# Performance work log

Measured on AMD Instinct MI355X. Metric: run time of the kernel, lower is better.

## Reference

```python
import jax, jax.numpy as jnp
import numpy as np

CANVAS = 512
SCORE_THR = 0.02
NMS_THR = 0.45
LVTOP = 1000      # cfg['lvtop'] for mm source
IMTOP = 200       # cfg['imtop']
NMS_PRE = 2000    # fixed pre-NMS candidate cap (static shape for jit)
NUM_CLASSES = 80
STRIDES = [8, 16, 32, 64, 128, 256, 512]
AR3 = [False, True, True, True, True, False, False]


def _make_priors():
    # get_scales(512): smallest=0.04, rmin=0.1, rmax=0.9, n=7
    smallest, rmin, rmax, n = 0.04, 0.1, 0.9, 7
    step = (rmax - rmin) / (n - 2)
    scales = [smallest] + [rmin + i * step for i in range(n)]
    sz = np.round(np.array(scales) * CANVAS).astype(np.int64)
    pr, lvlen = [], []
    for i, s in enumerate(STRIDES):
        fs = CANVAS // s
        ratios = [1.0, 2.0, 0.5] + ([3.0, 1.0 / 3.0] if AR3[i] else [])
        wh = [(sz[i] * np.sqrt(r), sz[i] / np.sqrt(r)) for r in ratios]
        extra = np.sqrt(float(sz[i]) * float(sz[i + 1]))  # sqrt(sz[i+1]/sz[i])*sz[i]
        wh.insert(1, (extra, extra))
        wh = np.array(wh, np.float32)            # [na, 2]
        xs = (np.arange(fs, dtype=np.float32) + 0.5) * s
        cx, cy = np.meshgrid(xs, xs)             # rows index y
        ctr = np.stack([cx, cy], -1)[:, :, None, :]  # [fs, fs, 1, 2]
        na = wh.shape[0]
        p = np.concatenate([np.broadcast_to(ctr, (fs, fs, na, 2)),
                            np.broadcast_to(wh, (fs, fs, na, 2))], -1).reshape(-1, 4)
        pr.append(p)
        lvlen.append(p.shape[0])
    return np.concatenate(pr).astype(np.float32), lvlen

PRIORS_NP, LVLEN = _make_priors()   # total 24564, lvlen=[16384,6144,1536,384,96,16,4]


def setup_inputs() -> dict:
    key = jax.random.key(0)
    k1, k2 = jax.random.split(key)
    A = PRIORS_NP.shape[0]
    cls_logits = jax.random.normal(k1, (4, A, NUM_CLASSES + 1), dtype=jnp.float32)
    reg = jax.random.normal(k2, (4, A, 4), dtype=jnp.float32)
    priors = jnp.asarray(PRIORS_NP)
    return {"cls_logits": cls_logits, "reg": reg, "priors": priors}


def _pairwise_iou(b):  # b: [K,4] xyxy
    area = (b[:, 2] - b[:, 0]) * (b[:, 3] - b[:, 1])
    lt = jnp.maximum(b[:, None, :2], b[None, :, :2])
    rb = jnp.minimum(b[:, None, 2:], b[None, :, 2:])
    wh = jnp.clip(rb - lt, 0.0)
    inter = wh[..., 0] * wh[..., 1]
    return inter / jnp.maximum(area[:, None] + area[None, :] - inter, 1e-6)


def _nms_keep(b):  # boxes sorted by descending score, class-offset applied
    m = _pairwise_iou(b) * jnp.triu(jnp.ones((NMS_PRE, NMS_PRE), b.dtype), 1)
    def body(sup, i):
        sup = sup | ((~sup[i]) & (m[i] > NMS_THR))
        return sup, None
    sup, _ = jax.lax.scan(body, jnp.zeros((NMS_PRE,), bool), jnp.arange(NMS_PRE))
    return ~sup


def reference(cls_logits, reg, priors):
    N = cls_logits.shape[0]
    C = NUM_CLASSES
    # softmax, background class is LAST (bckg_class_first=False for mm source)
    scr = jax.nn.softmax(cls_logits, axis=-1)[..., :-1]
    scr = jnp.where(scr > SCORE_THR, scr, 0.0)  # score threshold (fidx filter)
    # per-level top-k over flattened (anchor, class) pairs  [post.top_per_level]
    vals_l, anch_l, cls_l = [], [], []
    start = 0
    for lv in LVLEN:
        f = scr[:, start:start + lv, :].reshape(N, lv * C)
        k = min(LVTOP, lv * C)
        v, idx = jax.lax.top_k(f, k)
        vals_l.append(v)
        anch_l.append(start + idx // C)
        cls_l.append(idx % C)
        start += lv
    vals = jnp.concatenate(vals_l, 1)
    anch = jnp.concatenate(anch_l, 1)
    cls = jnp.concatenate(cls_l, 1)
    # fixed-size pre-NMS cap (static shapes under jit)
    v2, sel = jax.lax.top_k(vals, NMS_PRE)
    anch = jnp.take_along_axis(anch, sel, 1)
    cls = jnp.take_along_axis(cls, sel, 1)
    # decode boxes  [post.decode_boxes, mults=(0.1, 0.2), clamp=True]
    p = priors[anch]                                 # [N,K,4] cxcywh
    r = jnp.take_along_axis(reg, anch[..., None], 1)  # [N,K,4]
    cx = p[..., 0] + r[..., 0] * 0.1 * p[..., 2]
    cy = p[..., 1] + r[..., 1] * 0.1 * p[..., 3]
    w = p[..., 2] * jnp.exp(r[..., 2] * 0.2)
    h = p[..., 3] * jnp.exp(r[..., 3] * 0.2)
    boxes = jnp.stack([cx - w / 2, cy - h / 2, cx + w / 2, cy + h / 2], -1)
    boxes = jnp.clip(boxes, 0.0, float(CANVAS))
    # class-aware NMS via class offsets
    nb = boxes + cls.astype(boxes.dtype)[..., None] * (2.0 * CANVAS)
    keep = jax.vmap(_nms_keep)(nb)                   # [N,K] bool
    fs = jnp.where(keep & (v2 > 0), v2, 0.0)
    fv, fi = jax.lax.top_k(fs, IMTOP)                # imtop
    fb = jnp.take_along_axis(boxes, fi[..., None], 1)
    fc = jnp.take_along_axis(cls, fi, 1)
    fb = jnp.where(fv[..., None] > 0, fb, 0.0)
    return fb, fv, fc
```

## Files before the change

kernel.cpp:

```cpp
#include <hip/hip_runtime.h>
#include <hip/hip_bf16.h>
#include <math.h>

typedef unsigned long long u64;
typedef unsigned int u32;

#define A_TOTAL 24564
#define NCLS 80
#define NIMG 4
#define NPRE 2000
#define NLV 7
#define HBUCKETS 1024
#define BEXP_BASE 0x3CA3
#define TOTAL_G (NIMG * A_TOTAL)
#define FA 64
#define FT 256
#define NBLK_F ((TOTAL_G + FA - 1) / FA)
#define POOL_CAP_MAX 4096
#define CAPSEL 4608

__device__ __constant__ int c_klv[NLV] = {1000,1000,1000,1000,1000,1000,320};

#define WS_HIST      0
#define WS_MCOUNT    114688
#define WS_BCOUNT    114800
#define WS_ZERO_END  114912
#define WS_PCOUNT    114912
#define WS_CUTS      121056
#define WS_MAIN      121280
#define WS_BND       350656
#define WS_BOXES     1268160
#define WS_CLS       1396160
#define WS_SCORE     1428160
#define WS_MASK      1460160
#define WS_POOL      3508160

#define NZERO_W (WS_ZERO_END / 4)

__device__ inline u64 shfl_u64(u64 v, int src) {
  int lo = __shfl((int)(u32)(v & 0xFFFFFFFFULL), src);
  int hi = __shfl((int)(u32)(v >> 32), src);
  return ((u64)(u32)hi << 32) | (u32)lo;
}

__device__ inline int score_bucket(u32 bits) {
  int b = (int)(bits >> 16) - BEXP_BASE;
  return b < 0 ? 0 : (b > HBUCKETS - 1 ? HBUCKETS - 1 : b);
}

__device__ inline int level_of(int a) {
  return (a < 16384) ? 0 : (a < 22528) ? 1 : (a < 24064) ? 2 :
         (a < 24448) ? 3 : (a < 24544) ? 4 : (a < 24560) ? 5 : 6;
}

__global__ __launch_bounds__(256) void k_zero(u32* __restrict__ p) {
  int i = blockIdx.x * 256 + threadIdx.x;
  if (i < NZERO_W) p[i] = 0;
}

__device__ inline void wave_find_cut(const u32* __restrict__ h, int k, int lane,
                                     int& cx, int& cy) {
  u32 s = 0;
#pragma unroll
  for (int i = 0; i < 16; ++i) s += h[lane * 16 + i];
  u32 S = s;
#pragma unroll
  for (int o = 1; o < 64; o <<= 1) {
    u32 t = (u32)__shfl_down((int)S, o);
    if (lane + o < 64) S += t;
  }
  u32 total = (u32)__shfl((int)S, 0);
  if (total <= (u32)k) { cx = -1; cy = 0; return; }
  u64 bm = __ballot(S >= (u32)k);
  int L0 = 63 - (int)__clzll((long long)bm);
  u32 Sup = (u32)__shfl_down((int)S, 1);
  if (lane == 63) Sup = 0;
  int rcx = 0, rcy = 0;
  if (lane == L0) {
    u32 cum = Sup;
    for (int i = 15; i >= 0; --i) {
      u32 c = h[lane * 16 + i];
      if (cum + c >= (u32)k) { rcx = lane * 16 + i; rcy = k - (int)cum; break; }
      cum += c;
    }
  }
  cx = __shfl(rcx, L0);
  cy = __shfl(rcy, L0);
}

__global__ __launch_bounds__(FT) void k_fused(const float* __restrict__ logits,
                                              u32* __restrict__ histG,
                                              u64* __restrict__ pool,
                                              u32* __restrict__ pcount, int cap) {
  __shared__ float sx[FA * 81];
  __shared__ u32 sh[HBUCKETS];
  __shared__ int nm;
  int tid = threadIdx.x, bx = blockIdx.x;
  for (int b = tid; b < HBUCKETS; b += FT) sh[b] = 0;
  if (tid == 0) nm = 0;
  size_t base_f = (size_t)bx * (FA * 81);
  int cap4 = FA * 81 / 4;
  long long rem4 = ((long long)TOTAL_G * 81 - (long long)base_f) / 4;
  int n4 = (rem4 > cap4) ? cap4 : (int)rem4;
  const float4* src = (const float4*)(logits + base_f);
  float4* dst = (float4*)sx;
  for (int t = tid; t < n4; t += FT) dst[t] = src[t];
  __syncthreads();
  int la = tid >> 2, q = tid & 3;
  int g = bx * FA + la;
  bool valid = g < TOTAL_G;
  int g0 = bx * FA;
  int seg0 = (g0 / A_TOTAL) * NLV + level_of(g0 % A_TOTAL);
  int seg = seg0, a = 0;
  float e[20];
  float rt = 0.f;
  if (valid) {
    int img = g / A_TOTAL;
    a = g - img * A_TOTAL;
    seg = img * NLV + level_of(a);
    int rowoff = la * 81, c0 = q * 20;
    float mloc = sx[rowoff + c0];
#pragma unroll
    for (int i = 1; i < 20; ++i) mloc = fmaxf(mloc, sx[rowoff + c0 + i]);
    if (q == 3) mloc = fmaxf(mloc, sx[rowoff + 80]);
    float m = fmaxf(mloc, __shfl_xor(mloc, 1));
    m = fmaxf(m, __shfl_xor(m, 2));
    float tq = 0.f;
#pragma unroll
    for (int i = 0; i < 20; ++i) { e[i] = expf(sx[rowoff + c0 + i] - m); tq += e[i]; }
    if (q == 3) tq += expf(sx[rowoff + 80] - m);
    float t = tq + __shfl_xor(tq, 1);
    t = t + __shfl_xor(t, 2);
    rt = 1.0f / t;
  }
  int uniform = __syncthreads_and((int)(!valid || seg == seg0));
  if (valid) {
    u32* hdst = uniform ? sh : (histG + (size_t)seg * HBUCKETS);
    int c0 = q * 20;
    u32 wmask = 0;
#pragma unroll
    for (int i = 0; i < 20; ++i) {
      float s = e[i] * rt;
      if (s > 0.02f) wmask |= (1u << i);
    }
    int cnt = __popc(wmask);
    int basep = 0;
    if (cnt) basep = atomicAdd(&nm, cnt);
    while (wmask) {
      int i = __ffs(wmask) - 1;
      wmask &= wmask - 1;
      float s = e[i] * rt;
      u32 bits = __float_as_uint(s);
      atomicAdd(&hdst[score_bucket(bits)], 1u);
      if (basep < cap)
        pool[(size_t)bx * cap + basep] =
            ((u64)bits << 32) | (u64)(0xFFFFFFFFu - (u32)(a * NCLS + c0 + i));
      ++basep;
    }
  }
  __syncthreads();
  if (uniform) {
    u32* hseg = histG + (size_t)seg0 * HBUCKETS;
    for (int b = tid; b < HBUCKETS; b += FT) {
      u32 v = sh[b];
      if (v) atomicAdd(&hseg[b], v);
    }
  }
  if (tid == 0) pcount[bx] = (u32)nm;
}

__global__ __launch_bounds__(1024) void k_cuts(const u32* __restrict__ histG,
                                               int2* __restrict__ cutsG) {
  int wid = threadIdx.x >> 6, lane = threadIdx.x & 63;
  for (int seg = wid; seg < NIMG * NLV; seg += 16) {
    int cx, cy;
    wave_find_cut(histG + (size_t)seg * HBUCKETS, c_klv[seg % NLV], lane, cx, cy);
    if (lane == 0) cutsG[seg] = make_int2(cx, cy);
  }
}

__global__ __launch_bounds__(FT) void k_filter(const float* __restrict__ logits,
                                               const u64* __restrict__ pool,
                                               const u32* __restrict__ pcount,
                                               const int2* __restrict__ cutsG, int cap,
                                               u64* __restrict__ mainG, u32* __restrict__ mcount,
                                               u64* __restrict__ bndG, u32* __restrict__ bcount) {
  __shared__ float sx[FA * 81];
  __shared__ int2 scuts[NIMG * NLV];
  __shared__ u64 mk[1024]; __shared__ unsigned char msg_[1024];
  __shared__ u64 bkl[256]; __shared__ unsigned char bsg[256];
  __shared__ int nm, nb, cm[4], cb[4], basem[4], baseb[4], wm[4], wb[4];
  int tid = threadIdx.x, bx = blockIdx.x;
  if (tid < NIMG * NLV) scuts[tid] = cutsG[tid];
  if (tid < 4) { cm[tid] = 0; cb[tid] = 0; wm[tid] = 0; wb[tid] = 0; }
  if (tid == 0) { nm = 0; nb = 0; }
  int g0 = bx * FA;
  int img0 = g0 / A_TOTAL;
  int alo = g0 - img0 * A_TOTAL;
  int gN = g0 + FA - 1; if (gN > TOTAL_G - 1) gN = TOTAL_G - 1;
  int seg_lo = img0 * NLV + level_of(alo);
  int seg_hi = (gN / A_TOTAL) * NLV + level_of(gN % A_TOTAL);
  __syncthreads();
  int n = (int)pcount[bx];
  if (n <= cap) {
    for (int t = tid; t < n; t += FT) {
      u64 key = pool[(size_t)bx * cap + t];
      u32 bits = (u32)(key >> 32);
      u32 flat = 0xFFFFFFFFu - (u32)(key & 0xFFFFFFFFULL);
      int a = (int)(flat / NCLS);
      int img = (a >= alo) ? img0 : img0 + 1;
      int seg = img * NLV + level_of(a);
      int2 ct = scuts[seg];
      int bk = score_bucket(bits);
      int si = seg - seg_lo;
      if (ct.x < 0 || bk > ct.x) {
        int p = atomicAdd(&nm, 1);
        if (p < 1024) { mk[p] = key; msg_[p] = (unsigned char)si; atomicAdd(&cm[si], 1); }
        else { u32 pg = atomicAdd(&mcount[seg], 1u); if (pg < 1024) mainG[(size_t)seg * 1024 + pg] = key; }
      } else if (bk == ct.x) {
        int p = atomicAdd(&nb, 1);
        if (p < 256) { bkl[p] = key; bsg[p] = (unsigned char)si; atomicAdd(&cb[si], 1); }
        else { u32 pg = atomicAdd(&bcount[seg], 1u); if (pg < 4096) bndG[(size_t)seg * 4096 + pg] = key; }
      }
    }
  } else {
    size_t base_f = (size_t)bx * (FA * 81);
    int cap4 = FA * 81 / 4;
    long long rem4 = ((long long)TOTAL_G * 81 - (long long)base_f) / 4;
    int n4 = (rem4 > cap4) ? cap4 : (int)rem4;
    const float4* src = (const float4*)(logits + base_f);
    float4* dst = (float4*)sx;
    for (int t = tid; t < n4; t += FT) dst[t] = src[t];
    __syncthreads();
    int la = tid >> 2, q = tid & 3;
    int g = g0 + la;
    if (g < TOTAL_G) {
      int img = g / A_TOTAL;
      int a = g - img * A_TOTAL;
      int seg = img * NLV + level_of(a);
      int si = seg - seg_lo;
      int2 ct = scuts[seg];
      int rowoff = la * 81, c0 = q * 20;
      float mloc = sx[rowoff + c0];
#pragma unroll
      for (int i = 1; i < 20; ++i) mloc = fmaxf(mloc, sx[rowoff + c0 + i]);
      if (q == 3) mloc = fmaxf(mloc, sx[rowoff + 80]);
      float m = fmaxf(mloc, __shfl_xor(mloc, 1));
      m = fmaxf(m, __shfl_xor(m, 2));
      float tq = 0.f;
      float e[20];
#pragma unroll
      for (int i = 0; i < 20; ++i) { e[i] = expf(sx[rowoff + c0 + i] - m); tq += e[i]; }
      if (q == 3) tq += expf(sx[rowoff + 80] - m);
      float tt = tq + __shfl_xor(tq, 1);
      tt = tt + __shfl_xor(tt, 2);
      float rt = 1.0f / tt;
      for (int i = 0; i < 20; ++i) {
        float s = e[i] * rt;
        if (s > 0.02f) {
          u32 bits = __float_as_uint(s);
          int bk = score_bucket(bits);
          u64 key = ((u64)bits << 32) | (u64)(0xFFFFFFFFu - (u32)(a * NCLS + c0 + i));
          if (ct.x < 0 || bk > ct.x) {
            int p = atomicAdd(&nm, 1);
            if (p < 1024) { mk[p] = key; msg_[p] = (unsigned char)si; atomicAdd(&cm[si], 1); }
            else { u32 pg = atomicAdd(&mcount[seg], 1u); if (pg < 1024) mainG[(size_t)seg * 1024 + pg] = key; }
          } else if (bk == ct.x) {
            int p = atomicAdd(&nb, 1);
            if (p < 256) { bkl[p] = key; bsg[p] = (unsigned char)si; atomicAdd(&cb[si], 1); }
            else { u32 pg = atomicAdd(&bcount[seg], 1u); if (pg < 4096) bndG[(size_t)seg * 4096 + pg] = key; }
          }
        }
      }
    }
  }
  __syncthreads();
  if (tid <= seg_hi - seg_lo) {
    if (cm[tid] > 0) basem[tid] = (int)atomicAdd(&mcount[seg_lo + tid], (u32)cm[tid]);
    if (cb[tid] > 0) baseb[tid] = (int)atomicAdd(&bcount[seg_lo + tid], (u32)cb[tid]);
  }
  __syncthreads();
  int tm = nm < 1024 ? nm : 1024;
  for (int idx = tid; idx < tm; idx += FT) {
    int si = msg_[idx];
    int slot = atomicAdd(&wm[si], 1);
    int d = basem[si] + slot;
    if (d < 1024) mainG[(size_t)(seg_lo + si) * 1024 + d] = mk[idx];
  }
  int tb = nb < 256 ? nb : 256;
  for (int idx = tid; idx < tb; idx += FT) {
    int si = bsg[idx];
    int slot = atomicAdd(&wb[si], 1);
    int d = baseb[si] + slot;
    if (d < 4096) bndG[(size_t)(seg_lo + si) * 4096 + d] = bkl[idx];
  }
}

__device__ inline void bitonic_desc(u64* s, int n) {
  for (int k = 2; k <= n; k <<= 1)
    for (int j = k >> 1; j > 0; j >>= 1) {
      __syncthreads();
      for (int i = threadIdx.x; i < n; i += blockDim.x) {
        int l = i ^ j;
        if (l > i) {
          u64 a = s[i], b = s[l];
          if (((i & k) == 0) ? (a < b) : (a > b)) { s[i] = b; s[l] = a; }
        }
      }
    }
  __syncthreads();
}

__global__ __launch_bounds__(1024) void k_refine(const u32* __restrict__ histG,
                                                 const u64* __restrict__ bndG,
                                                 const u32* __restrict__ bcount,
                                                 u64* __restrict__ mainG, u32* __restrict__ mcount) {
  int seg = blockIdx.x;
  __shared__ int sh_cx, sh_cy;
  __shared__ u64 s[4096];
  int tid = threadIdx.x, lane = tid & 63;
  if (tid < 64) {
    int cx, cy;
    wave_find_cut(histG + (size_t)seg * HBUCKETS, c_klv[seg % NLV], lane, cx, cy);
    if (lane == 0) { sh_cx = cx; sh_cy = cy; }
  }
  __syncthreads();
  if (sh_cx < 0) return;
  int m = (int)bcount[seg]; if (m > 4096) m = 4096;
  int n = 64; while (n < m) n <<= 1;
  for (int t = tid; t < n; t += 1024)
    s[t] = (t < m) ? bndG[(size_t)seg * 4096 + t] : 0ULL;
  bitonic_desc(s, n);
  int kp = sh_cy; if (kp > m) kp = m;
  int base = (int)mcount[seg];
  for (int t = tid; t < kp; t += 1024) {
    int p = base + t;
    if (p < 1024) mainG[(size_t)seg * 1024 + p] = s[t];
  }
  __syncthreads();
  if (tid == 0) {
    int nb = base + kp;
    mcount[seg] = (u32)(nb > 1024 ? 1024 : nb);
  }
}

__global__ __launch_bounds__(1024) void k_gsel(const u32* __restrict__ histG,
                                               const u64* __restrict__ mainG,
                                               const u32* __restrict__ mcount,
                                               const float4* __restrict__ priors,
                                               const float4* __restrict__ reg,
                                               float4* __restrict__ boxesG,
                                               int* __restrict__ clsG,
                                               float* __restrict__ scoreG) {
  int img = blockIdx.x;
  int tid = threadIdx.x, wid = tid >> 6, lane = tid & 63;
  __shared__ u32 H[HBUCKETS];
  __shared__ u32 cntb[HBUCKETS];
  __shared__ u32 Sarr[HBUCKETS];
  __shared__ u32 cnt2[HBUCKETS];
  __shared__ u64 sel[CAPSEL];
  __shared__ int lcx[NLV], lcy[NLV];
  __shared__ int sh_gx, sh_gy, sh_cC, sh_cand, sh_sgx;
  if (tid == 0) { sh_cC = 0; sh_cand = 0; sh_sgx = -1; }
  if (wid < NLV) {
    int cx, cy;
    wave_find_cut(histG + (size_t)(img * NLV + wid) * HBUCKETS, c_klv[wid], lane, cx, cy);
    if (lane == 0) { lcx[wid] = cx; lcy[wid] = cy; }
  }
  __syncthreads();
  for (int b = tid; b < HBUCKETS; b += 1024) {
    u32 acc = 0;
#pragma unroll
    for (int l = 0; l < NLV; ++l) {
      u32 h = histG[(size_t)(img * NLV + l) * HBUCKETS + b];
      int cx = lcx[l];
      if (cx < 0 || b > cx) acc += h;
      else if (b == cx) acc += (u32)lcy[l];
    }
    H[b] = acc;
    cntb[b] = 0;
    cnt2[b] = 0;
  }
  __syncthreads();
  if (wid == 0) {
    int gx, gy;
    wave_find_cut(H, NPRE, lane, gx, gy);
    if (lane == 0) { sh_gx = gx; sh_gy = gy; }
  }
  __syncthreads();
  int gx = sh_gx, gy = sh_gy;
  int mcap[NLV];
#pragma unroll
  for (int l = 0; l < NLV; ++l) { int c = (int)mcount[img * NLV + l]; mcap[l] = c > 1024 ? 1024 : c; }
  for (int l = 0; l < NLV; ++l)
    for (int t = tid; t < mcap[l]; t += 1024) {
      u64 key = mainG[(size_t)(img * NLV + l) * 1024 + t];
      int b = score_bucket((u32)(key >> 32));
      if (gx < 0 || b > gx) atomicAdd(&cntb[b], 1u);
      else if (b == gx) atomicAdd(&sh_cC, 1);
    }
  __syncthreads();
  for (int b = tid; b < HBUCKETS; b += 1024) Sarr[b] = cntb[b];
  __syncthreads();
  {
    u32* A = Sarr; u32* B = H;
    for (int o = 1; o < HBUCKETS; o <<= 1) {
      for (int b = tid; b < HBUCKETS; b += 1024)
        B[b] = A[b] + ((b + o < HBUCKETS) ? A[b + o] : 0u);
      __syncthreads();
      u32* tmp = A; A = B; B = tmp;
    }
  }
  int cA = (int)Sarr[0];
  int cC = sh_cC;
  int cand = (gx >= 0) ? cC : 0;
  int sgx = -1;
  if (gx >= 0 && cA + cC > CAPSEL) {
    for (int b = tid; b < HBUCKETS; b += 1024) H[b] = 0;
    __syncthreads();
    for (int l = 0; l < NLV; ++l)
      for (int t = tid; t < mcap[l]; t += 1024) {
        u64 key = mainG[(size_t)(img * NLV + l) * 1024 + t];
        u32 bits = (u32)(key >> 32);
        if (score_bucket(bits) == gx) atomicAdd(&H[(bits >> 6) & 1023], 1u);
      }
    __syncthreads();
    if (wid == 0) {
      int a1, a2;
      wave_find_cut(H, gy, lane, a1, a2);
      if (lane == 0) sh_sgx = a1;
    }
    __syncthreads();
    sgx = sh_sgx;
    if (sgx >= 0) {
      for (int s2 = tid; s2 < HBUCKETS; s2 += 1024)
        if (s2 >= sgx) { u32 v = H[s2]; if (v) atomicAdd(&sh_cand, (int)v); }
      __syncthreads();
      cand = sh_cand;
    }
    if (cA + cand > CAPSEL) cand = CAPSEL - cA;
  }
  __syncthreads();
  for (int l = 0; l < NLV; ++l)
    for (int t = tid; t < mcap[l]; t += 1024) {
      u64 key = mainG[(size_t)(img * NLV + l) * 1024 + t];
      u32 bits = (u32)(key >> 32);
      int b = score_bucket(bits);
      bool inc = false; int segbase = 0, seglen = 0;
      if (gx < 0 || b > gx) {
        inc = true; segbase = (int)(Sarr[b] - cntb[b]); seglen = (int)cntb[b];
      } else if (b == gx) {
        inc = (sgx < 0) || ((int)((bits >> 6) & 1023) >= sgx);
        segbase = (int)Sarr[b]; seglen = cand;
      }
      if (inc) {
        int slot = (int)atomicAdd(&cnt2[b], 1u);
        if (slot < seglen) sel[segbase + slot] = key;
      }
    }
  __syncthreads();
  int total = cA + cand;
  u64 myk[5]; int myp[5];
#pragma unroll
  for (int it = 0; it < 5; ++it) {
    int t = tid + it * 1024;
    myp[it] = -1; myk[it] = 0;
    if (t < total) {
      u64 key = sel[t];
      u32 bits = (u32)(key >> 32);
      int b = score_bucket(bits);
      int segbase, seglen;
      if (gx >= 0 && b == gx) { segbase = (int)Sarr[b]; seglen = cand; }
      else { segbase = (int)(Sarr[b] - cntb[b]); seglen = (int)cntb[b]; }
      int r = 0;
      for (int u = 0; u < seglen; ++u) r += (sel[segbase + u] > key) ? 1 : 0;
      myk[it] = key; myp[it] = segbase + r;
    }
  }
  __syncthreads();
#pragma unroll
  for (int it = 0; it < 5; ++it) if (myp[it] >= 0) sel[myp[it]] = myk[it];
  __syncthreads();
  for (int t = tid; t < NPRE; t += 1024) {
    u64 key = (t < total) ? sel[t] : 0ULL;
    float4 bx = make_float4(0.f, 0.f, 0.f, 0.f);
    int c = -1;
    float sc = 0.f;
    if (key != 0ULL) {
      sc = __uint_as_float((u32)(key >> 32));
      u32 flat = 0xFFFFFFFFu - (u32)(key & 0xFFFFFFFFULL);
      int a = (int)(flat / NCLS);
      c = (int)(flat % NCLS);
      float4 p = priors[a];
      float4 r = reg[(size_t)img * A_TOTAL + a];
      float cx = p.x + (r.x * 0.1f) * p.z;
      float cy = p.y + (r.y * 0.1f) * p.w;
      float w = p.z * expf(r.z * 0.2f);
      float h = p.w * expf(r.w * 0.2f);
      bx.x = fminf(fmaxf(cx - w * 0.5f, 0.f), 512.f);
      bx.y = fminf(fmaxf(cy - h * 0.5f, 0.f), 512.f);
      bx.z = fminf(fmaxf(cx + w * 0.5f, 0.f), 512.f);
      bx.w = fminf(fmaxf(cy + h * 0.5f, 0.f), 512.f);
    }
    boxesG[(size_t)img * NPRE + t] = bx;
    clsG[(size_t)img * NPRE + t] = c;
    scoreG[(size_t)img * NPRE + t] = sc;
  }
}

__global__ __launch_bounds__(256) void k_mask(const float4* __restrict__ boxesG,
                                              const int* __restrict__ clsG,
                                              u64* __restrict__ maskG) {
  __shared__ float4 lb[NPRE];
  __shared__ int lc[NPRE];
  int img = blockIdx.x / 500;
  int rb = (blockIdx.x % 500) * 4;
  for (int t = threadIdx.x; t < NPRE; t += 256) {
    lb[t] = boxesG[(size_t)img * NPRE + t];
    lc[t] = clsG[(size_t)img * NPRE + t];
  }
  __syncthreads();
  int w = threadIdx.x >> 6, lane = threadIdx.x & 63;
  int i = rb + w;
  float4 bi = lb[i];
  int ci = lc[i];
  float ai = (bi.z - bi.x) * (bi.w - bi.y);
  u64* mrow = maskG + ((size_t)img * NPRE + i) * 32;
  for (int ch = 0; ch < 32; ++ch) {
    int j = ch * 64 + lane;
    bool pred = false;
    if (j < NPRE && j > i) {
      if (lc[j] == ci) {
        float4 bj = lb[j];
        float xx1 = fmaxf(bi.x, bj.x), yy1 = fmaxf(bi.y, bj.y);
        float xx2 = fminf(bi.z, bj.z), yy2 = fminf(bi.w, bj.w);
        float ww = fmaxf(xx2 - xx1, 0.f), hh = fmaxf(yy2 - yy1, 0.f);
        float inter = ww * hh;
        float aj = (bj.z - bj.x) * (bj.w - bj.y);
        float iou = inter / fmaxf(ai + aj - inter, 1e-6f);
        pred = iou > 0.45f;
      }
    }
    u64 word = __ballot(pred);
    if (lane == 0) mrow[ch] = word;
  }
}

__global__ __launch_bounds__(256) void k_scanfinal(const u64* __restrict__ maskG,
                                                   const float4* __restrict__ boxesG,
                                                   const int* __restrict__ clsG,
                                                   const float* __restrict__ scoreG,
                                                   float* __restrict__ out) {
  int img = blockIdx.x;
  int tid = threadIdx.x;
  __shared__ u64 sh_remv[32];
  __shared__ u32 keptList[216];
  __shared__ int sh_cnt, sh_done;
  __shared__ int kpref[257];
  __shared__ unsigned short S[NPRE];
  if (tid == 0) { sh_cnt = 0; sh_done = 0; }
  __syncthreads();
  if (tid < 64) {
    int lane = tid;
    int wl = lane & 31;
    const u64* M = maskG + (size_t)img * NPRE * 32;
    u64 remv = 0;
    u64 cur[16], nxt[16];
    int cnt = 0;
#pragma unroll
    for (int r = 0; r < 16; ++r) cur[r] = M[(size_t)r * 32 + wl];
    int t = 0;
    for (; t < 125; ++t) {
      if (t < 124) {
#pragma unroll
        for (int r = 0; r < 16; ++r) nxt[r] = M[(size_t)((t + 1) * 16 + r) * 32 + wl];
      }
#pragma unroll
      for (int r = 0; r < 16; ++r) {
        int i = t * 16 + r;
        u64 rm = shfl_u64(remv, i >> 6);
        if (!((rm >> (i & 63)) & 1ULL)) {
          remv |= cur[r];
          if (lane == 0 && cnt < 216) keptList[cnt] = (u32)i;
          ++cnt;
        }
      }
#pragma unroll
      for (int r = 0; r < 16; ++r) cur[r] = nxt[r];
      if (cnt >= 200) { ++t; break; }
    }
    if (lane == 0) sh_cnt = cnt < 216 ? cnt : 216;
    if (t >= 125) {
      if (lane == 0) sh_done = 1;
      if (lane < 32) sh_remv[lane] = remv;
    }
  }
  __syncthreads();
  int nK = sh_cnt;
  if (sh_done && nK < 200) {
    int base = tid * 8;
    bool sb[8];
    int scnt = 0;
#pragma unroll
    for (int e = 0; e < 8; ++e) {
      int i = base + e;
      bool sup = (i < NPRE) && ((sh_remv[i >> 6] >> (i & 63)) & 1ULL);
      sb[e] = sup;
      scnt += sup ? 1 : 0;
    }
    kpref[tid + 1] = scnt;
    if (tid == 0) kpref[0] = 0;
    __syncthreads();
    if (tid == 0) {
      int acc = 0;
      for (int t = 1; t <= 256; ++t) { acc += kpref[t]; kpref[t] = acc; }
    }
    __syncthreads();
    int sp = kpref[tid];
#pragma unroll
    for (int e = 0; e < 8; ++e) {
      int i = base + e;
      if (i < NPRE && sb[e]) S[sp++] = (unsigned short)i;
    }
    __syncthreads();
    if (tid < 200) {
      float fv = 0.f;
      float4 fb = make_float4(0.f, 0.f, 0.f, 0.f);
      int fc;
      if (tid < nK) {
        int idx = (int)keptList[tid];
        fv = scoreG[(size_t)img * NPRE + idx];
        fb = boxesG[(size_t)img * NPRE + idx];
        fc = clsG[(size_t)img * NPRE + idx];
      } else {
        int idx = S[tid - nK];
        fc = clsG[(size_t)img * NPRE + idx];
      }
      float* fbo = out + (size_t)img * 800 + tid * 4;
      fbo[0] = fb.x; fbo[1] = fb.y; fbo[2] = fb.z; fbo[3] = fb.w;
      out[3200 + (size_t)img * 200 + tid] = fv;
      out[4000 + (size_t)img * 200 + tid] = (float)fc;
    }
  } else {
    if (tid < 200) {
      int idx = (int)keptList[tid];
      float fv = scoreG[(size_t)img * NPRE + idx];
      float4 fb = boxesG[(size_t)img * NPRE + idx];
      int fc = clsG[(size_t)img * NPRE + idx];
      float* fbo = out + (size_t)img * 800 + tid * 4;
      fbo[0] = fb.x; fbo[1] = fb.y; fbo[2] = fb.z; fbo[3] = fb.w;
      out[3200 + (size_t)img * 200 + tid] = fv;
      out[4000 + (size_t)img * 200 + tid] = (float)fc;
    }
  }
}

extern "C" void kernel_launch(void* const* d_in, const int* in_sizes, int n_in,
                              void* d_out, int out_size, void* d_ws, size_t ws_size,
                              hipStream_t stream) {
  const float* logits = (const float*)d_in[0];
  const float4* reg = (const float4*)d_in[1];
  const float4* priors = (const float4*)d_in[2];
  char* ws = (char*)d_ws;
  u32* hist = (u32*)(ws + WS_HIST);
  u32* mcount = (u32*)(ws + WS_MCOUNT);
  u32* bcount = (u32*)(ws + WS_BCOUNT);
  u32* pcount = (u32*)(ws + WS_PCOUNT);
  int2* cuts = (int2*)(ws + WS_CUTS);
  u64* mainL = (u64*)(ws + WS_MAIN);
  u64* bndL = (u64*)(ws + WS_BND);
  float4* boxes = (float4*)(ws + WS_BOXES);
  int* cls = (int*)(ws + WS_CLS);
  float* score = (float*)(ws + WS_SCORE);
  u64* mask = (u64*)(ws + WS_MASK);
  u64* pool = (u64*)(ws + WS_POOL);

  size_t avail = ws_size > (size_t)WS_POOL ? ws_size - (size_t)WS_POOL : 0;
  int cap = (int)(avail / ((size_t)NBLK_F * 8));
  if (cap > POOL_CAP_MAX) cap = POOL_CAP_MAX;

  k_zero<<<(NZERO_W + 255) / 256, 256, 0, stream>>>((u32*)d_ws);
  k_fused<<<NBLK_F, FT, 0, stream>>>(logits, hist, pool, pcount, cap);
  k_cuts<<<1, 1024, 0, stream>>>(hist, cuts);
  k_filter<<<NBLK_F, FT, 0, stream>>>(logits, pool, pcount, cuts, cap,
                                      mainL, mcount, bndL, bcount);
  k_refine<<<28, 1024, 0, stream>>>(hist, bndL, bcount, mainL, mcount);
  k_gsel<<<NIMG, 1024, 0, stream>>>(hist, mainL, mcount, priors, reg, boxes, cls, score);
  k_mask<<<NIMG * 500, 256, 0, stream>>>(boxes, cls, mask);
  k_scanfinal<<<NIMG, 256, 0, stream>>>(mask, boxes, cls, score, (float*)d_out);
}
```

Measured before the change: 123.3 us.

## Fold cut computation into filter blocks and read logits directly without LDS staging

Removes the single-block k_cuts launch. Each k_filter block now computes the histogram cuts for its own one to four segments with per-wave scans and keeps them in shared memory. It also drops the shared-memory staging of logits in k_fused and in the k_filter fallback, so each thread reads its 20 logits straight from global memory through a shared score20 helper. This saves one kernel launch and a serial stage. In exchange, every filter block re-reads the histograms, and the direct global loads are strided per thread instead of coalesced float4 copies.

```diff
diff --git a/kernel.cpp b/kernel.cpp
--- a/kernel.cpp
+++ b/kernel.cpp
@@ -26,7 +26,6 @@
 #define WS_BCOUNT    114800
 #define WS_ZERO_END  114912
 #define WS_PCOUNT    114912
-#define WS_CUTS      121056
 #define WS_MAIN      121280
 #define WS_BND       350656
 #define WS_BOXES     1268160
@@ -56,6 +55,28 @@
 __global__ __launch_bounds__(256) void k_zero(u32* __restrict__ p) {
   int i = blockIdx.x * 256 + threadIdx.x;
   if (i < NZERO_W) p[i] = 0;
+}
+
+__device__ inline void score20(const float* __restrict__ logits, int g, int q,
+                               float (&e)[20], float& rt) {
+  const float* row = logits + (size_t)g * 81;
+  float x[20];
+#pragma unroll
+  for (int i = 0; i < 20; ++i) x[i] = row[q * 20 + i];
+  float x80 = (q == 3) ? row[80] : 0.f;
+  float mloc = x[0];
+#pragma unroll
+  for (int i = 1; i < 20; ++i) mloc = fmaxf(mloc, x[i]);
+  if (q == 3) mloc = fmaxf(mloc, x80);
+  float m = fmaxf(mloc, __shfl_xor(mloc, 1));
+  m = fmaxf(m, __shfl_xor(m, 2));
+  float tq = 0.f;
+#pragma unroll
+  for (int i = 0; i < 20; ++i) { e[i] = expf(x[i] - m); tq += e[i]; }
+  if (q == 3) tq += expf(x80 - m);
+  float t = tq + __shfl_xor(tq, 1);
+  t = t + __shfl_xor(t, 2);
+  rt = 1.0f / t;
 }
 
 __device__ inline void wave_find_cut(const u32* __restrict__ h, int k, int lane,
@@ -92,20 +113,11 @@
                                               u32* __restrict__ histG,
                                               u64* __restrict__ pool,
                                               u32* __restrict__ pcount, int cap) {
-  __shared__ float sx[FA * 81];
   __shared__ u32 sh[HBUCKETS];
   __shared__ int nm;
   int tid = threadIdx.x, bx = blockIdx.x;
   for (int b = tid; b < HBUCKETS; b += FT) sh[b] = 0;
   if (tid == 0) nm = 0;
-  size_t base_f = (size_t)bx * (FA * 81);
-  int cap4 = FA * 81 / 4;
-  long long rem4 = ((long long)TOTAL_G * 81 - (long long)base_f) / 4;
-  int n4 = (rem4 > cap4) ? cap4 : (int)rem4;
-  const float4* src = (const float4*)(logits + base_f);
-  float4* dst = (float4*)sx;
-  for (int t = tid; t < n4; t += FT) dst[t] = src[t];
-  __syncthreads();
   int la = tid >> 2, q = tid & 3;
   int g = bx * FA + la;
   bool valid = g < TOTAL_G;
@@ -118,20 +130,7 @@
     int img = g / A_TOTAL;
     a = g - img * A_TOTAL;
     seg = img * NLV + level_of(a);
-    int rowoff = la * 81, c0 = q * 20;
-    float mloc = sx[rowoff + c0];
-#pragma unroll
-    for (int i = 1; i < 20; ++i) mloc = fmaxf(mloc, sx[rowoff + c0 + i]);
-    if (q == 3) mloc = fmaxf(mloc, sx[rowoff + 80]);
-    float m = fmaxf(mloc, __shfl_xor(mloc, 1));
-    m = fmaxf(m, __shfl_xor(m, 2));
-    float tq = 0.f;
-#pragma unroll
-    for (int i = 0; i < 20; ++i) { e[i] = expf(sx[rowoff + c0 + i] - m); tq += e[i]; }
-    if (q == 3) tq += expf(sx[rowoff + 80] - m);
-    float t = tq + __shfl_xor(tq, 1);
-    t = t + __shfl_xor(t, 2);
-    rt = 1.0f / t;
+    score20(logits, g, q, e, rt);
   }
   int uniform = __syncthreads_and((int)(!valid || seg == seg0));
   if (valid) {
@@ -169,29 +168,17 @@
   if (tid == 0) pcount[bx] = (u32)nm;
 }
 
-__global__ __launch_bounds__(1024) void k_cuts(const u32* __restrict__ histG,
-                                               int2* __restrict__ cutsG) {
-  int wid = threadIdx.x >> 6, lane = threadIdx.x & 63;
-  for (int seg = wid; seg < NIMG * NLV; seg += 16) {
-    int cx, cy;
-    wave_find_cut(histG + (size_t)seg * HBUCKETS, c_klv[seg % NLV], lane, cx, cy);
-    if (lane == 0) cutsG[seg] = make_int2(cx, cy);
-  }
-}
-
 __global__ __launch_bounds__(FT) void k_filter(const float* __restrict__ logits,
                                                const u64* __restrict__ pool,
                                                const u32* __restrict__ pcount,
-                                               const int2* __restrict__ cutsG, int cap,
+                                               const u32* __restrict__ histG, int cap,
                                                u64* __restrict__ mainG, u32* __restrict__ mcount,
                                                u64* __restrict__ bndG, u32* __restrict__ bcount) {
-  __shared__ float sx[FA * 81];
-  __shared__ int2 scuts[NIMG * NLV];
+  __shared__ int lcx4[4];
   __shared__ u64 mk[1024]; __shared__ unsigned char msg_[1024];
   __shared__ u64 bkl[256]; __shared__ unsigned char bsg[256];
   __shared__ int nm, nb, cm[4], cb[4], basem[4], baseb[4], wm[4], wb[4];
   int tid = threadIdx.x, bx = blockIdx.x;
-  if (tid < NIMG * NLV) scuts[tid] = cutsG[tid];
   if (tid < 4) { cm[tid] = 0; cb[tid] = 0; wm[tid] = 0; wb[tid] = 0; }
   if (tid == 0) { nm = 0; nb = 0; }
   int g0 = bx * FA;
@@ -200,6 +187,14 @@
   int gN = g0 + FA - 1; if (gN > TOTAL_G - 1) gN = TOTAL_G - 1;
   int seg_lo = img0 * NLV + level_of(alo);
   int seg_hi = (gN / A_TOTAL) * NLV + level_of(gN % A_TOTAL);
+  int nseg = seg_hi - seg_lo + 1;
+  int wid = tid >> 6, lane = tid & 63;
+  if (wid < nseg) {
+    int cx, cy;
+    wave_find_cut(histG + (size_t)(seg_lo + wid) * HBUCKETS,
+                  c_klv[(seg_lo + wid) % NLV], lane, cx, cy);
+    if (lane == 0) lcx4[wid] = cx;
+  }
   __syncthreads();
   int n = (int)pcount[bx];
   if (n <= cap) {
@@ -210,28 +205,20 @@
       int a = (int)(flat / NCLS);
       int img = (a >= alo) ? img0 : img0 + 1;
       int seg = img * NLV + level_of(a);
-      int2 ct = scuts[seg];
+      int si = seg - seg_lo;
+      int ctx = lcx4[si];
       int bk = score_bucket(bits);
-      int si = seg - seg_lo;
-      if (ct.x < 0 || bk > ct.x) {
+      if (ctx < 0 || bk > ctx) {
         int p = atomicAdd(&nm, 1);
         if (p < 1024) { mk[p] = key; msg_[p] = (unsigned char)si; atomicAdd(&cm[si], 1); }
         else { u32 pg = atomicAdd(&mcount[seg], 1u); if (pg < 1024) mainG[(size_t)seg * 1024 + pg] = key; }
-      } else if (bk == ct.x) {
+      } else if (bk == ctx) {
         int p = atomicAdd(&nb, 1);
         if (p < 256) { bkl[p] = key; bsg[p] = (unsigned char)si; atomicAdd(&cb[si], 1); }
         else { u32 pg = atomicAdd(&bcount[seg], 1u); if (pg < 4096) bndG[(size_t)seg * 4096 + pg] = key; }
       }
     }
   } else {
-    size_t base_f = (size_t)bx * (FA * 81);
-    int cap4 = FA * 81 / 4;
-    long long rem4 = ((long long)TOTAL_G * 81 - (long long)base_f) / 4;
-    int n4 = (rem4 > cap4) ? cap4 : (int)rem4;
-    const float4* src = (const float4*)(logits + base_f);
-    float4* dst = (float4*)sx;
-    for (int t = tid; t < n4; t += FT) dst[t] = src[t];
-    __syncthreads();
     int la = tid >> 2, q = tid & 3;
     int g = g0 + la;
     if (g < TOTAL_G) {
@@ -239,33 +226,22 @@
       int a = g - img * A_TOTAL;
       int seg = img * NLV + level_of(a);
       int si = seg - seg_lo;
-      int2 ct = scuts[seg];
-      int rowoff = la * 81, c0 = q * 20;
-      float mloc = sx[rowoff + c0];
-#pragma unroll
-      for (int i = 1; i < 20; ++i) mloc = fmaxf(mloc, sx[rowoff + c0 + i]);
-      if (q == 3) mloc = fmaxf(mloc, sx[rowoff + 80]);
-      float m = fmaxf(mloc, __shfl_xor(mloc, 1));
-      m = fmaxf(m, __shfl_xor(m, 2));
-      float tq = 0.f;
+      int ctx = lcx4[si];
       float e[20];
-#pragma unroll
-      for (int i = 0; i < 20; ++i) { e[i] = expf(sx[rowoff + c0 + i] - m); tq += e[i]; }
-      if (q == 3) tq += expf(sx[rowoff + 80] - m);
-      float tt = tq + __shfl_xor(tq, 1);
-      tt = tt + __shfl_xor(tt, 2);
-      float rt = 1.0f / tt;
+      float rt;
+      score20(logits, g, q, e, rt);
+      int c0 = q * 20;
       for (int i = 0; i < 20; ++i) {
         float s = e[i] * rt;
         if (s > 0.02f) {
           u32 bits = __float_as_uint(s);
           int bk = score_bucket(bits);
           u64 key = ((u64)bits << 32) | (u64)(0xFFFFFFFFu - (u32)(a * NCLS + c0 + i));
-          if (ct.x < 0 || bk > ct.x) {
+          if (ctx < 0 || bk > ctx) {
             int p = atomicAdd(&nm, 1);
             if (p < 1024) { mk[p] = key; msg_[p] = (unsigned char)si; atomicAdd(&cm[si], 1); }
             else { u32 pg = atomicAdd(&mcount[seg], 1u); if (pg < 1024) mainG[(size_t)seg * 1024 + pg] = key; }
-          } else if (bk == ct.x) {
+          } else if (bk == ctx) {
             int p = atomicAdd(&nb, 1);
             if (p < 256) { bkl[p] = key; bsg[p] = (unsigned char)si; atomicAdd(&cb[si], 1); }
             else { u32 pg = atomicAdd(&bcount[seg], 1u); if (pg < 4096) bndG[(size_t)seg * 4096 + pg] = key; }
@@ -275,7 +251,7 @@
     }
   }
   __syncthreads();
-  if (tid <= seg_hi - seg_lo) {
+  if (tid < nseg) {
     if (cm[tid] > 0) basem[tid] = (int)atomicAdd(&mcount[seg_lo + tid], (u32)cm[tid]);
     if (cb[tid] > 0) baseb[tid] = (int)atomicAdd(&bcount[seg_lo + tid], (u32)cb[tid]);
   }
@@ -666,7 +642,6 @@
   u32* mcount = (u32*)(ws + WS_MCOUNT);
   u32* bcount = (u32*)(ws + WS_BCOUNT);
   u32* pcount = (u32*)(ws + WS_PCOUNT);
-  int2* cuts = (int2*)(ws + WS_CUTS);
   u64* mainL = (u64*)(ws + WS_MAIN);
   u64* bndL = (u64*)(ws + WS_BND);
   float4* boxes = (float4*)(ws + WS_BOXES);
@@ -681,8 +656,7 @@
 
   k_zero<<<(NZERO_W + 255) / 256, 256, 0, stream>>>((u32*)d_ws);
   k_fused<<<NBLK_F, FT, 0, stream>>>(logits, hist, pool, pcount, cap);
-  k_cuts<<<1, 1024, 0, stream>>>(hist, cuts);
-  k_filter<<<NBLK_F, FT, 0, stream>>>(logits, pool, pcount, cuts, cap,
+  k_filter<<<NBLK_F, FT, 0, stream>>>(logits, pool, pcount, hist, cap,
                                       mainL, mcount, bndL, bcount);
   k_refine<<<28, 1024, 0, stream>>>(hist, bndL, bcount, mainL, mcount);
   k_gsel<<<NIMG, 1024, 0, stream>>>(hist, mainL, mcount, priors, reg, boxes, cls, score);
```

Measured after the change: 113.5 us. 7.9% less time.
